# Kernel optimization log

Measured on AMD Instinct MI355X. Metric: run time of the kernel, lower is better.

## Reference

```python
import jax, jax.numpy as jnp
import numpy as np

B, S, D = 1, 2048, 1024
H, HD = 16, 64            # heads, head_dim = D // H
TEN, ED, K = 32, 128, 8   # experts, expert_dim, top_k
DS = 2048                 # shared expert dim
THETA = 10000.0
EPS = 1e-6
RSF = 2.5                 # routed_scaling_factor


def setup_inputs() -> dict:
    key = jax.random.key(0)
    ks = jax.random.split(key, 12)
    s = 0.02
    return {
        "x_input": jax.random.normal(ks[0], (B, S, D), jnp.float32),
        "indices": jax.random.randint(ks[1], (B * S, K), 0, TEN, dtype=jnp.int32),
        "values": jax.random.normal(ks[2], (B * S, K), jnp.float32),
        "w_attn": jax.random.normal(ks[3], (D, 3 * D), jnp.float32) * s,
        "w_attn_o": jax.random.normal(ks[4], (D, D), jnp.float32) * s,
        "attn_norm_w": jnp.ones((D,), jnp.float32),
        "ffn_norm_w": jnp.ones((D,), jnp.float32),
        "ffn_experts": jax.random.normal(ks[5], (3, TEN, D, ED), jnp.float32) * s,
        "keys_w": jax.random.normal(ks[6], (D, TEN), jnp.float32) * s,
        "w_up": jax.random.normal(ks[7], (D, 2 * DS), jnp.float32) * s,
        "w_down": jax.random.normal(ks[8], (DS, D), jnp.float32) * s,
    }


def rmsnorm(x, w):
    return x * jax.lax.rsqrt(jnp.mean(x * x, -1, keepdims=True) + EPS) * w


def l2norm(x):
    # F.normalize(x, dim=-1, eps=EPS)
    n = jnp.sqrt(jnp.sum(x * x, -1, keepdims=True))
    return x / jnp.maximum(n, EPS)


def rope(x):
    # x: [B, H, S, HD]
    t = jnp.arange(x.shape[2], dtype=jnp.float32)
    inv = (1.0 / THETA) ** (jnp.arange(0, HD, 2, dtype=jnp.float32) / HD)
    f = jnp.outer(t, inv)[None, None]  # [1,1,S,HD//2]
    cos, sin = jnp.cos(f), jnp.sin(f)
    x1, x2 = jnp.split(x, 2, -1)
    return jnp.concatenate([x1 * cos + x2 * sin, -x1 * sin + x2 * cos], -1)


def reference(x_input, indices, values, w_attn, w_attn_o, attn_norm_w,
              ffn_norm_w, ffn_experts, keys_w, w_up, w_down):
    # ---- attention block ----
    x = rmsnorm(x_input, attn_norm_w)
    qkv = x @ w_attn  # [B,S,3D]
    xq, xk, xv = jnp.split(qkv, 3, -1)
    to_heads = lambda t: t.reshape(B, S, H, HD).transpose(0, 2, 1, 3)  # b h s a
    xq, xk, xv = to_heads(xq), to_heads(xk), to_heads(xv)
    xq, xk = l2norm(xq), l2norm(xk)  # qk_norm
    xq, xk = rope(xq), rope(xk)
    scores = jnp.einsum('bhqd,bhkd->bhqk', xq, xk) / jnp.sqrt(jnp.float32(HD))
    causal = jnp.tril(jnp.ones((S, S), bool))
    scores = jnp.where(causal, scores, jnp.finfo(scores.dtype).min)
    probs = jax.nn.softmax(scores, -1)
    x_attn = jnp.einsum('bhqk,bhkd->bhqd', probs, xv)
    x_attn = x_attn.transpose(0, 2, 1, 3).reshape(B, S, D)
    x_attn_o = x_attn @ w_attn_o
    x_ffn_input = x_attn_o + x_input

    # ---- router ----
    x_ffn = rmsnorm(x_ffn_input, ffn_norm_w)
    xf = x_ffn.reshape(B * S, D)
    logits = xf @ keys_w  # [T, TEN]
    token_values = jnp.take_along_axis(logits, indices, -1)  # [T, K]
    gates = jax.nn.sigmoid(values + token_values) * RSF

    # ---- grouped-GEMM expert dispatch (dense equivalent: combine is linear in score) ----
    T = B * S
    w_route = jnp.zeros((T, TEN), xf.dtype).at[jnp.arange(T)[:, None], indices].add(gates)
    g = jnp.einsum('td,edh->teh', xf, ffn_experts[0])
    u = jnp.einsum('td,edh->teh', xf, ffn_experts[1])
    h = jax.nn.silu(g) * u * w_route[:, :, None]
    y = jnp.einsum('teh,edh->td', h, ffn_experts[2]).reshape(B, S, D)

    # ---- shared expert (SwiGLU FFN) ----
    x1, x2 = jnp.split(x_ffn @ w_up, 2, -1)
    y_shared = (jax.nn.silu(x1) * x2) @ w_down
    y = y + y_shared
    return y + x_ffn_input
```

## Files before the change

### kernel.cpp

```cpp
#include <hip/hip_runtime.h>
#include <math.h>

#define TOKENS 2048
#define DIM 1024
#define NHEADS 16
#define HEADDIM 64
#define NEXP 32
#define EDIM 128
#define TOPK 8
#define DSHARED 2048
#define RSF_ 2.5f
#define EPS_ 1e-6f

using bf8  = __attribute__((ext_vector_type(8))) short;
using f32x4 = __attribute__((ext_vector_type(4))) float;

__device__ __forceinline__ short f2bf(float f) {
    unsigned u = __float_as_uint(f);
    unsigned r = (u + 0x7fffu + ((u >> 16) & 1u)) >> 16;
    return (short)r;
}
__device__ __forceinline__ float bf2f(short s) {
    return __uint_as_float(((unsigned)(unsigned short)s) << 16);
}

__device__ __forceinline__ void async16(const short* g, const short* l) {
    __builtin_amdgcn_global_load_lds(
        (const __attribute__((address_space(1))) void*)(unsigned long long)g,
        (__attribute__((address_space(3))) void*)(unsigned)(unsigned long long)l,
        16, 0, 0);
}

__global__ __launch_bounds__(256) void rmsnorm_kernel(const float* __restrict__ x,
                                                      const float* __restrict__ w,
                                                      short* __restrict__ out) {
    int row = blockIdx.x;
    const float* xr = x + (long long)row * DIM;
    int t = threadIdx.x;
    float4 xv = ((const float4*)xr)[t];
    float ss = xv.x*xv.x + xv.y*xv.y + xv.z*xv.z + xv.w*xv.w;
    #pragma unroll
    for (int off = 32; off; off >>= 1) ss += __shfl_down(ss, off);
    __shared__ float warps[4];
    if ((t & 63) == 0) warps[t >> 6] = ss;
    __syncthreads();
    float tot = warps[0] + warps[1] + warps[2] + warps[3];
    float scale = rsqrtf(tot / (float)DIM + EPS_);
    float4 wv = ((const float4*)w)[t];
    short4 o;
    o.x = f2bf(xv.x * scale * wv.x);
    o.y = f2bf(xv.y * scale * wv.y);
    o.z = f2bf(xv.z * scale * wv.z);
    o.w = f2bf(xv.w * scale * wv.w);
    ((short4*)(out + (long long)row * DIM))[t] = o;
}

__global__ __launch_bounds__(256) void tconv(const float* __restrict__ in, long long sin,
                                             short* __restrict__ out, long long sout,
                                             int K, int N) {
    in  += (long long)blockIdx.z * sin;
    out += (long long)blockIdx.z * sout;
    __shared__ float t[32][33];
    int n0 = blockIdx.x * 32, k0 = blockIdx.y * 32;
    int tx = threadIdx.x & 31, ty = threadIdx.x >> 5;
    #pragma unroll
    for (int r = ty; r < 32; r += 8)
        t[r][tx] = in[(long long)(k0 + r) * N + n0 + tx];
    __syncthreads();
    #pragma unroll
    for (int r = ty; r < 32; r += 8)
        out[(long long)(n0 + r) * K + k0 + tx] = f2bf(t[tx][r]);
}

__global__ void w2conv(const float* __restrict__ in, short* __restrict__ out) {
    long long i = (long long)blockIdx.x * 256 + threadIdx.x;
    int e = (int)(i >> 17);
    int d = (int)(i >> 7) & 1023;
    int h = (int)(i & 127);
    out[(long long)d * (NEXP * EDIM) + e * EDIM + h] = f2bf(in[i]);
}

__global__ __launch_bounds__(256) void guconv(const float* __restrict__ ex,
                                              short* __restrict__ wgu) {
    int z = blockIdx.z;
    int e = z & 31, hf = z >> 5;
    const float* in = ex + (long long)hf * (NEXP * DIM * EDIM) + (long long)e * (DIM * EDIM);
    short* outp = wgu + (long long)e * (256 * 1024);
    __shared__ float t[32][33];
    int n0 = blockIdx.x * 32, k0 = blockIdx.y * 32;
    int tx = threadIdx.x & 31, ty = threadIdx.x >> 5;
    #pragma unroll
    for (int r = ty; r < 32; r += 8)
        t[r][tx] = in[(long long)(k0 + r) * EDIM + n0 + tx];
    __syncthreads();
    #pragma unroll
    for (int r = ty; r < 32; r += 8) {
        int c = n0 + r;
        int rr = ((c >> 4) << 5) + hf * 16 + (c & 15);
        outp[(long long)rr * 1024 + k0 + tx] = f2bf(t[tx][r]);
    }
}

__global__ __launch_bounds__(256) void upconv(const float* __restrict__ in,
                                              short* __restrict__ outp) {
    __shared__ float t[32][33];
    int n0 = blockIdx.x * 32, k0 = blockIdx.y * 32;
    int tx = threadIdx.x & 31, ty = threadIdx.x >> 5;
    #pragma unroll
    for (int r = ty; r < 32; r += 8)
        t[r][tx] = in[(long long)(k0 + r) * (2 * DSHARED) + n0 + tx];
    __syncthreads();
    #pragma unroll
    for (int r = ty; r < 32; r += 8) {
        int n = n0 + r;
        int hf = n >> 11, c2 = n & 2047;
        int rr = ((c2 >> 7) << 8) + (((c2 & 127) >> 4) << 5) + hf * 16 + (c2 & 15);
        outp[(long long)rr * 1024 + k0 + tx] = f2bf(t[tx][r]);
    }
}

template<int MODE>
__global__ __launch_bounds__(256) void gemm_bf16(const short* __restrict__ A, int lda, long long sA,
                                                 const short* __restrict__ Bt, int ldb, long long sBt,
                                                 void* __restrict__ Cv, int ldc, long long sC,
                                                 int M, int N, int K) {
    int koff = 0, Ksub = K;
    if (MODE >= 3) {
        Ksub = K / gridDim.z;
        koff = blockIdx.z * Ksub;
    } else {
        A  += (long long)blockIdx.z * sA;
        Bt += (long long)blockIdx.z * sBt;
    }
    float* Cf = (float*)Cv;
    short* Cs = (short*)Cv;
    Cf += (long long)blockIdx.z * sC;
    Cs += (long long)blockIdx.z * sC;
    const int m0 = blockIdx.y * 128, n0 = blockIdx.x * 128;
    __shared__ short As[128 * 64];
    __shared__ short Bs[128 * 64];
    const int tid = threadIdx.x, lane = tid & 63, w = tid >> 6;
    const int wm = (w >> 1) * 64, wn = (w & 1) * 64;
    const int drow = lane >> 3;
    const int dcol = ((lane & 7) ^ drow) * 8;
    const short* ag = A + (long long)(m0 + w * 32 + drow) * lda + koff + dcol;
    const short* bg = Bt + (long long)(n0 + w * 32 + drow) * ldb + koff + dcol;
    const short* lA = As + w * 32 * 64;
    const short* lB = Bs + w * 32 * 64;
    f32x4 acc[4][4];
    #pragma unroll
    for (int i = 0; i < 4; ++i)
        #pragma unroll
        for (int j = 0; j < 4; ++j) { f32x4 z = {0.f, 0.f, 0.f, 0.f}; acc[i][j] = z; }
    const int ra = lane & 15, quad = lane >> 4;
    const int fs0 = ((quad + 0) ^ (ra & 7)) * 8;
    const int fs1 = ((quad + 4) ^ (ra & 7)) * 8;
    for (int k0 = 0; k0 < Ksub; k0 += 64) {
        #pragma unroll
        for (int c = 0; c < 4; ++c) {
            async16(ag + (long long)(c * 8) * lda + k0, lA + c * 512);
            async16(bg + (long long)(c * 8) * ldb + k0, lB + c * 512);
        }
        __syncthreads();
        #pragma unroll
        for (int h = 0; h < 2; ++h) {
            const int fs = h ? fs1 : fs0;
            bf8 af[4], bfv[4];
            #pragma unroll
            for (int i = 0; i < 4; ++i) af[i]  = *(const bf8*)(As + (wm + i * 16 + ra) * 64 + fs);
            #pragma unroll
            for (int j = 0; j < 4; ++j) bfv[j] = *(const bf8*)(Bs + (wn + j * 16 + ra) * 64 + fs);
            #pragma unroll
            for (int i = 0; i < 4; ++i)
                #pragma unroll
                for (int j = 0; j < 4; ++j)
                    acc[i][j] = __builtin_amdgcn_mfma_f32_16x16x32_bf16(af[i], bfv[j], acc[i][j], 0, 0, 0);
        }
        __syncthreads();
    }
    const int cr = quad * 4, cc = ra;
    #pragma unroll
    for (int i = 0; i < 4; ++i) {
        #pragma unroll
        for (int r = 0; r < 4; ++r) {
            int row = m0 + wm + i * 16 + cr + r;
            long long base = (long long)row * ldc + n0 + wn + cc;
            #pragma unroll
            for (int j = 0; j < 4; ++j) {
                float v = acc[i][j][r];
                if (MODE == 2) Cs[base + j * 16] = f2bf(v);
                if (MODE == 3) Cf[base + j * 16] = v;
                if (MODE == 4) Cf[base + j * 16] = Cf[base + j * 16] + v;
            }
        }
    }
}

template<bool SCALED>
__global__ __launch_bounds__(256) void gemm_act(const short* __restrict__ A, int lda,
                                                const short* __restrict__ Bt, long long sBt,
                                                short* __restrict__ Ct, int ldct,
                                                const float* __restrict__ wr) {
    const short* Bp = Bt + (long long)blockIdx.z * sBt + (long long)blockIdx.x * (256 * 1024);
    const int cb = (blockIdx.z * gridDim.x + blockIdx.x) * 128;
    const int m0 = blockIdx.y * 64;
    __shared__ short As[2][64 * 64];
    __shared__ short Bs[2][256 * 64];
    const int tid = threadIdx.x, lane = tid & 63, w = tid >> 6;
    const int wm = (w >> 1) * 32, wn = (w & 1) * 128;
    const int drow = lane >> 3;
    const int dcol = ((lane & 7) ^ drow) * 8;
    const short* ag = A + (long long)(m0 + w * 16 + drow) * lda + dcol;
    const short* bg = Bp + (long long)(w * 64 + drow) * 1024 + dcol;
    f32x4 acc[2][8];
    #pragma unroll
    for (int i = 0; i < 2; ++i)
        #pragma unroll
        for (int j = 0; j < 8; ++j) { f32x4 z = {0.f, 0.f, 0.f, 0.f}; acc[i][j] = z; }
    const int ra = lane & 15, quad = lane >> 4;
    const int fs0 = ((quad + 0) ^ (ra & 7)) * 8;
    const int fs1 = ((quad + 4) ^ (ra & 7)) * 8;

    {
        const short* lA = As[0] + w * 16 * 64;
        const short* lB = Bs[0] + w * 64 * 64;
        async16(ag, lA);
        async16(ag + (long long)8 * lda, lA + 512);
        #pragma unroll
        for (int c = 0; c < 8; ++c)
            async16(bg + (long long)(c * 8) * 1024, lB + c * 512);
    }
    int cur = 0;
    for (int k0 = 0; k0 < 1024; k0 += 64) {
        __syncthreads();
        if (k0 + 64 < 1024) {
            const int nxt = cur ^ 1;
            const short* lA = As[nxt] + w * 16 * 64;
            const short* lB = Bs[nxt] + w * 64 * 64;
            async16(ag + k0 + 64, lA);
            async16(ag + (long long)8 * lda + k0 + 64, lA + 512);
            #pragma unroll
            for (int c = 0; c < 8; ++c)
                async16(bg + (long long)(c * 8) * 1024 + k0 + 64, lB + c * 512);
        }
        const short* cA = As[cur];
        const short* cB = Bs[cur];
        #pragma unroll
        for (int h = 0; h < 2; ++h) {
            const int fs = h ? fs1 : fs0;
            bf8 af0 = *(const bf8*)(cA + (wm + ra) * 64 + fs);
            bf8 af1 = *(const bf8*)(cA + (wm + 16 + ra) * 64 + fs);
            #pragma unroll
            for (int j = 0; j < 8; ++j) {
                bf8 bv = *(const bf8*)(cB + (wn + j * 16 + ra) * 64 + fs);
                acc[0][j] = __builtin_amdgcn_mfma_f32_16x16x32_bf16(af0, bv, acc[0][j], 0, 0, 0);
                acc[1][j] = __builtin_amdgcn_mfma_f32_16x16x32_bf16(af1, bv, acc[1][j], 0, 0, 0);
            }
        }
        cur ^= 1;
    }
    #pragma unroll
    for (int i = 0; i < 2; ++i)
        #pragma unroll
        for (int r = 0; r < 4; ++r) {
            int token = m0 + wm + i * 16 + quad * 4 + r;
            float scale = SCALED ? wr[token * NEXP + blockIdx.z] : 1.0f;
            #pragma unroll
            for (int jp = 0; jp < 4; ++jp) {
                float g = acc[i][2 * jp][r];
                float u = acc[i][2 * jp + 1][r];
                float v = g / (1.0f + __expf(-g)) * u * scale;
                Ct[(long long)token * ldct + cb + wn / 2 + jp * 16 + ra] = f2bf(v);
            }
        }
}

__global__ void combine4(const float* __restrict__ slices, const float* __restrict__ add,
                         float* __restrict__ dst) {
    long long i = (long long)blockIdx.x * 256 + threadIdx.x;
    const long long S4 = (long long)TOKENS * DIM / 4;
    float4 s = ((const float4*)add)[i];
    #pragma unroll
    for (int c = 0; c < 4; ++c) {
        float4 p = ((const float4*)slices)[c * S4 + i];
        s.x += p.x; s.y += p.y; s.z += p.z; s.w += p.w;
    }
    ((float4*)dst)[i] = s;
}

__global__ __launch_bounds__(256) void combine_rms(const float* __restrict__ slices,
                                                   const float* __restrict__ add,
                                                   const float* __restrict__ w,
                                                   float* __restrict__ xffn,
                                                   short* __restrict__ xf) {
    int row = blockIdx.x, t = threadIdx.x;
    long long i = (long long)row * 256 + t;
    const long long S4 = (long long)TOKENS * DIM / 4;
    float4 s = ((const float4*)add)[i];
    #pragma unroll
    for (int c = 0; c < 4; ++c) {
        float4 p = ((const float4*)slices)[c * S4 + i];
        s.x += p.x; s.y += p.y; s.z += p.z; s.w += p.w;
    }
    ((float4*)xffn)[i] = s;
    float ss = s.x*s.x + s.y*s.y + s.z*s.z + s.w*s.w;
    #pragma unroll
    for (int off = 32; off; off >>= 1) ss += __shfl_down(ss, off);
    __shared__ float warps[4];
    if ((t & 63) == 0) warps[t >> 6] = ss;
    __syncthreads();
    float tot = warps[0] + warps[1] + warps[2] + warps[3];
    float scale = rsqrtf(tot / (float)DIM + EPS_);
    float4 wv = ((const float4*)w)[t];
    short4 o;
    o.x = f2bf(s.x * scale * wv.x);
    o.y = f2bf(s.y * scale * wv.y);
    o.z = f2bf(s.z * scale * wv.z);
    o.w = f2bf(s.w * scale * wv.w);
    ((short4*)(xf + (long long)row * DIM))[t] = o;
}

__global__ __launch_bounds__(256) void qkv_post(const short* __restrict__ qkv,
                                                short* __restrict__ q,
                                                short* __restrict__ k) {
    int lane = threadIdx.x & 63;
    int sh = blockIdx.x * 4 + (threadIdx.x >> 6);
    int s = sh >> 4;
    int h = sh & 15;
    const short* base = qkv + (long long)s * 3 * DIM;
    float qv = bf2f(base[h * HEADDIM + lane]);
    float kv = bf2f(base[DIM + h * HEADDIM + lane]);
    float qs = qv * qv, ks = kv * kv;
    #pragma unroll
    for (int off = 32; off; off >>= 1) {
        qs += __shfl_xor(qs, off);
        ks += __shfl_xor(ks, off);
    }
    qv /= fmaxf(sqrtf(qs), EPS_);
    kv /= fmaxf(sqrtf(ks), EPS_);
    int i = lane & 31;
    float f = (float)s * powf(10000.0f, -(float)i / 32.0f);
    float c = cosf(f), sn = sinf(f);
    float qo = __shfl_xor(qv, 32);
    float ko = __shfl_xor(kv, 32);
    float sgn = (lane < 32) ? sn : -sn;
    float qr = qv * c + qo * sgn;
    float kr = kv * c + ko * sgn;
    long long o = ((long long)h * TOKENS + s) * HEADDIM + lane;
    q[o] = f2bf(qr);
    k[o] = f2bf(kr);
}

__global__ __launch_bounds__(256) void vtrans(const short* __restrict__ qkv,
                                              short* __restrict__ vt) {
    int h = blockIdx.z;
    int s0 = blockIdx.x * 32, d0 = blockIdx.y * 32;
    __shared__ short t[32][34];
    int tx = threadIdx.x & 31, ty = threadIdx.x >> 5;
    #pragma unroll
    for (int r = ty; r < 32; r += 8)
        t[r][tx] = qkv[(long long)(s0 + r) * (3 * DIM) + 2 * DIM + h * HEADDIM + d0 + tx];
    __syncthreads();
    #pragma unroll
    for (int r = ty; r < 32; r += 8)
        vt[((long long)h * HEADDIM + d0 + r) * TOKENS + s0 + tx] = t[tx][r];
}

#define PLD 68
__global__ __launch_bounds__(256) void attn_kernel(const short* __restrict__ q,
                                                   const short* __restrict__ k,
                                                   const short* __restrict__ vt,
                                                   float* __restrict__ Oacc,
                                                   float* __restrict__ lacc) {
    const int w = threadIdx.x >> 6, lane = threadIdx.x & 63;
    const int col = lane & 15, quad = lane >> 4;
    const int head = blockIdx.x / 80;
    const int t = blockIdx.x % 80;
    int qb, ch;
    if (t < 8)       { qb = t;                ch = 0; }
    else if (t < 24) { qb = 8 + (t - 8) / 2;  ch = (t - 8) % 2; }
    else if (t < 48) { qb = 16 + (t - 24) / 3; ch = (t - 24) % 3; }
    else             { qb = 24 + (t - 48) / 4; ch = (t - 48) % 4; }
    const int nch = qb / 8 + 1;
    const int ntk = qb + 1;
    const int per = (ntk + nch - 1) / nch;
    const int t0 = ch * per;
    const int t1 = (t0 + per < ntk) ? t0 + per : ntk;
    const int qbase = qb * 64 + w * 16;
    __shared__ short Ks[64 * 64];
    __shared__ short Vs[64 * 64];
    __shared__ short Ps[4 * 16 * PLD];
    short* Pw = Ps + w * 16 * PLD;
    const short* kh = k + (long long)head * TOKENS * HEADDIM;
    const short* vh = vt + (long long)head * HEADDIM * TOKENS;
    const int r8 = lane >> 3;
    const int sw = ((lane & 7) ^ r8) * 8;
    bf8 qf[2];
    #pragma unroll
    for (int ks = 0; ks < 2; ++ks)
        qf[ks] = *(const bf8*)(q + ((long long)head * TOKENS + qbase + col) * HEADDIM + ks * 32 + quad * 8);
    const int fo0 = (((0 * 4) + quad) ^ (col & 7)) * 8;
    const int fo1 = (((1 * 4) + quad) ^ (col & 7)) * 8;
    f32x4 o_[4];
    float l_[4];
    #pragma unroll
    for (int n = 0; n < 4; ++n) { f32x4 z = {0.f, 0.f, 0.f, 0.f}; o_[n] = z; }
    #pragma unroll
    for (int r = 0; r < 4; ++r) l_[r] = 0.f;
    for (int kt = t0; kt < t1; ++kt) {
        const int j0 = kt * 64;
        #pragma unroll
        for (int c = 0; c < 2; ++c) {
            int row = w * 16 + c * 8 + r8;
            async16(kh + (long long)(j0 + row) * HEADDIM + sw, Ks + (w * 16 + c * 8) * 64 + lane * 8);
            async16(vh + (long long)row * TOKENS + j0 + sw, Vs + (w * 16 + c * 8) * 64 + lane * 8);
        }
        __syncthreads();
        f32x4 sacc[4];
        #pragma unroll
        for (int n = 0; n < 4; ++n) { f32x4 z = {0.f, 0.f, 0.f, 0.f}; sacc[n] = z; }
        #pragma unroll
        for (int ks = 0; ks < 2; ++ks) {
            const int fo = ks ? fo1 : fo0;
            #pragma unroll
            for (int nt = 0; nt < 4; ++nt) {
                bf8 kf = *(const bf8*)(Ks + (nt * 16 + col) * 64 + fo);
                sacc[nt] = __builtin_amdgcn_mfma_f32_16x16x32_bf16(qf[ks], kf, sacc[nt], 0, 0, 0);
            }
        }
        const bool diag = (j0 + 64 > qbase);
        #pragma unroll
        for (int nt = 0; nt < 4; ++nt)
            #pragma unroll
            for (int r = 0; r < 4; ++r) {
                float p = __expf(sacc[nt][r] * 0.125f);
                if (diag && (j0 + nt * 16 + col > qbase + quad * 4 + r)) p = 0.f;
                l_[r] += p;
                Pw[(quad * 4 + r) * PLD + nt * 16 + col] = f2bf(p);
            }
        #pragma unroll
        for (int ks = 0; ks < 2; ++ks) {
            bf8 pf = *(const bf8*)(Pw + col * PLD + ks * 32 + quad * 8);
            const int fo = ks ? fo1 : fo0;
            #pragma unroll
            for (int nt = 0; nt < 4; ++nt) {
                bf8 vf = *(const bf8*)(Vs + (nt * 16 + col) * 64 + fo);
                o_[nt] = __builtin_amdgcn_mfma_f32_16x16x32_bf16(pf, vf, o_[nt], 0, 0, 0);
            }
        }
        __syncthreads();
    }
    float* Oc = Oacc + (long long)ch * (TOKENS * DIM);
    #pragma unroll
    for (int r = 0; r < 4; ++r) {
        int row = qbase + quad * 4 + r;
        float* op = Oc + (long long)row * DIM + head * HEADDIM;
        #pragma unroll
        for (int nt = 0; nt < 4; ++nt)
            op[nt * 16 + col] = o_[nt][r];
        float l = l_[r];
        #pragma unroll
        for (int off = 1; off < 16; off <<= 1) l += __shfl_xor(l, off);
        if (col == 0) lacc[ch * (TOKENS * NHEADS) + row * NHEADS + head] = l;
    }
}

__global__ void attn_norm(const float* __restrict__ Oacc, const float* __restrict__ lacc,
                          short* __restrict__ xo) {
    long long i = (long long)blockIdx.x * 256 + threadIdx.x;
    int row = (int)(i >> 10), col = (int)(i & 1023);
    int nch = (row >> 9) + 1;
    int head = col >> 6;
    float so = 0.f, sl = 0.f;
    for (int c = 0; c < nch; ++c) {
        so += Oacc[(long long)c * (TOKENS * DIM) + i];
        sl += lacc[c * (TOKENS * NHEADS) + row * NHEADS + head];
    }
    xo[i] = f2bf(so / sl);
}

__global__ __launch_bounds__(256) void router_kernel(const short* __restrict__ xf,
                                                     const float* __restrict__ keys_w,
                                                     const int* __restrict__ idx,
                                                     const float* __restrict__ vals,
                                                     float* __restrict__ w_route) {
    int t = blockIdx.x;
    int tid = threadIdx.x;
    int e = tid & 31, c = tid >> 5;
    const short* xr = xf + (long long)t * DIM;
    float p = 0.f;
    for (int j = 0; j < 128; ++j)
        p += bf2f(xr[c * 128 + j]) * keys_w[(c * 128 + j) * NEXP + e];
    __shared__ float part[8][32];
    part[c][e] = p;
    __syncthreads();
    if (tid < NEXP) {
        float lg = 0.f;
        #pragma unroll
        for (int cc = 0; cc < 8; ++cc) lg += part[cc][tid];
        part[0][tid] = lg;
    }
    __syncthreads();
    __shared__ float gate_s[TOPK];
    __shared__ int idx_s[TOPK];
    if (tid < TOPK) {
        int ii = idx[t * TOPK + tid];
        float g = vals[t * TOPK + tid] + part[0][ii];
        gate_s[tid] = (1.0f / (1.0f + __expf(-g))) * RSF_;
        idx_s[tid] = ii;
    }
    __syncthreads();
    if (tid < NEXP) {
        float wr = 0.f;
        #pragma unroll
        for (int kk = 0; kk < TOPK; ++kk)
            if (idx_s[kk] == tid) wr += gate_s[kk];
        w_route[(long long)t * NEXP + tid] = wr;
    }
}

extern "C" void kernel_launch(void* const* d_in, const int* in_sizes, int n_in,
                              void* d_out, int out_size, void* d_ws, size_t ws_size,
                              hipStream_t stream) {
    (void)in_sizes; (void)n_in; (void)out_size; (void)ws_size;
    const float* x_input     = (const float*)d_in[0];
    const int*   indices     = (const int*)d_in[1];
    const float* values      = (const float*)d_in[2];
    const float* w_attn      = (const float*)d_in[3];
    const float* w_attn_o    = (const float*)d_in[4];
    const float* attn_norm_w = (const float*)d_in[5];
    const float* ffn_norm_w  = (const float*)d_in[6];
    const float* ffn_experts = (const float*)d_in[7];
    const float* keys_w      = (const float*)d_in[8];
    const float* w_up        = (const float*)d_in[9];
    const float* w_down      = (const float*)d_in[10];
    float* out = (float*)d_out;
    float* ws  = (float*)d_ws;

    const long long M1 = 1024 * 1024;
    const long long SLICE = (long long)TOKENS * DIM;
    float* xffn    = ws + 0 * M1;
    short* xa_bf   = (short*)(ws + 4 * M1);
    short* xf_bf   = (short*)(ws + 4 * M1 + M1 / 2);
    short* xattn_bf= (short*)(ws + 5 * M1);
    float* w_route = ws + 5 * M1 + M1 / 2;
    float* Oacc    = ws + 6 * M1;
    float* lacc    = ws + 14 * M1;
    short* qh_bf   = (short*)(ws + 15 * M1);
    short* kh_bf   = (short*)(ws + 15 * M1 + M1 / 2);
    short* vt_bf   = (short*)(ws + 16 * M1);
    short* wattn_t = (short*)(ws + 17 * M1);
    short* wattno_t= (short*)(ws + 18 * M1 + M1 / 2);
    short* qkv_bf  = (short*)(ws + 21 * M1);
    float* oslice  = ws + 6 * M1;
    short* wgu     = (short*)(ws + 6 * M1);
    short* h_bf    = (short*)(ws + 10 * M1);
    short* w2t     = (short*)(ws + 14 * M1);
    float* yslice  = ws + 16 * M1;
    short* wupt    = (short*)(ws + 6 * M1);
    short* hs_bf   = (short*)(ws + 8 * M1);
    short* wdownt  = (short*)(ws + 10 * M1);

    tconv<<<dim3(3072 / 32, DIM / 32, 1), 256, 0, stream>>>(w_attn, 0, wattn_t, 0, DIM, 3 * DIM);
    rmsnorm_kernel<<<TOKENS, 256, 0, stream>>>(x_input, attn_norm_w, xa_bf);
    gemm_bf16<2><<<dim3(3072 / 128, TOKENS / 128, 1), 256, 0, stream>>>(
        xa_bf, DIM, 0, wattn_t, DIM, 0, qkv_bf, 3 * DIM, 0, TOKENS, 3 * DIM, DIM);
    qkv_post<<<(TOKENS * NHEADS) / 4, 256, 0, stream>>>(qkv_bf, qh_bf, kh_bf);
    vtrans<<<dim3(TOKENS / 32, HEADDIM / 32, NHEADS), 256, 0, stream>>>(qkv_bf, vt_bf);
    attn_kernel<<<NHEADS * 80, 256, 0, stream>>>(qh_bf, kh_bf, vt_bf, Oacc, lacc);
    attn_norm<<<(TOKENS * DIM) / 256, 256, 0, stream>>>(Oacc, lacc, xattn_bf);
    tconv<<<dim3(DIM / 32, DIM / 32, 1), 256, 0, stream>>>(w_attn_o, 0, wattno_t, 0, DIM, DIM);
    gemm_bf16<3><<<dim3(DIM / 128, TOKENS / 128, 4), 256, 0, stream>>>(
        xattn_bf, DIM, 0, wattno_t, DIM, 0, oslice, DIM, SLICE, TOKENS, DIM, DIM);
    combine_rms<<<TOKENS, 256, 0, stream>>>(oslice, x_input, ffn_norm_w, xffn, xf_bf);

    router_kernel<<<TOKENS, 256, 0, stream>>>(xf_bf, keys_w, indices, values, w_route);
    guconv<<<dim3(EDIM / 32, DIM / 32, 2 * NEXP), 256, 0, stream>>>(ffn_experts, wgu);
    gemm_act<true><<<dim3(1, TOKENS / 64, NEXP), 256, 0, stream>>>(
        xf_bf, DIM, wgu, 256 * 1024, h_bf, NEXP * EDIM, w_route);
    w2conv<<<(NEXP * DIM * EDIM) / 256, 256, 0, stream>>>(
        ffn_experts + 2LL * NEXP * DIM * EDIM, w2t);
    gemm_bf16<3><<<dim3(DIM / 128, TOKENS / 128, 4), 256, 0, stream>>>(
        h_bf, NEXP * EDIM, 0, w2t, NEXP * EDIM, 0, yslice, DIM, SLICE, TOKENS, DIM, NEXP * EDIM);

    upconv<<<dim3((2 * DSHARED) / 32, DIM / 32, 1), 256, 0, stream>>>(w_up, wupt);
    gemm_act<false><<<dim3((2 * DSHARED) / 256, TOKENS / 64, 1), 256, 0, stream>>>(
        xf_bf, DIM, wupt, 0, hs_bf, DSHARED, nullptr);
    tconv<<<dim3(DIM / 32, DSHARED / 32, 1), 256, 0, stream>>>(w_down, 0, wdownt, 0, DSHARED, DIM);
    gemm_bf16<4><<<dim3(DIM / 128, TOKENS / 128, 4), 256, 0, stream>>>(
        hs_bf, DSHARED, 0, wdownt, DSHARED, 0, yslice, DIM, SLICE, TOKENS, DIM, DSHARED);

    combine4<<<(TOKENS * DIM) / 1024, 256, 0, stream>>>(yslice, xffn, out);
}
```

Measured before the change: 412.5 us.

## Double-buffer LDS tiles in bf16 GEMM to overlap loads with MFMA

Shared memory tiles for A and B become two-stage ping-pong buffers. The first tile is prefetched before the loop, and each iteration issues the async load for the next K-tile right after the barrier, then computes on the current tile. This hides global-to-LDS latency behind MFMA work and removes one barrier per iteration. In exchange, LDS use per block doubles to 64KB, which can lower occupancy.

```diff
diff --git a/kernel.cpp b/kernel.cpp
--- a/kernel.cpp
+++ b/kernel.cpp
@@ -137,16 +137,14 @@
     Cf += (long long)blockIdx.z * sC;
     Cs += (long long)blockIdx.z * sC;
     const int m0 = blockIdx.y * 128, n0 = blockIdx.x * 128;
-    __shared__ short As[128 * 64];
-    __shared__ short Bs[128 * 64];
+    __shared__ short As[2][128 * 64];
+    __shared__ short Bs[2][128 * 64];
     const int tid = threadIdx.x, lane = tid & 63, w = tid >> 6;
     const int wm = (w >> 1) * 64, wn = (w & 1) * 64;
     const int drow = lane >> 3;
     const int dcol = ((lane & 7) ^ drow) * 8;
     const short* ag = A + (long long)(m0 + w * 32 + drow) * lda + koff + dcol;
     const short* bg = Bt + (long long)(n0 + w * 32 + drow) * ldb + koff + dcol;
-    const short* lA = As + w * 32 * 64;
-    const short* lB = Bs + w * 32 * 64;
     f32x4 acc[4][4];
     #pragma unroll
     for (int i = 0; i < 4; ++i)
@@ -155,28 +153,46 @@
     const int ra = lane & 15, quad = lane >> 4;
     const int fs0 = ((quad + 0) ^ (ra & 7)) * 8;
     const int fs1 = ((quad + 4) ^ (ra & 7)) * 8;
+
+    {
+        const short* lA = As[0] + w * 32 * 64;
+        const short* lB = Bs[0] + w * 32 * 64;
+        #pragma unroll
+        for (int c = 0; c < 4; ++c) {
+            async16(ag + (long long)(c * 8) * lda, lA + c * 512);
+            async16(bg + (long long)(c * 8) * ldb, lB + c * 512);
+        }
+    }
+    int cur = 0;
     for (int k0 = 0; k0 < Ksub; k0 += 64) {
-        #pragma unroll
-        for (int c = 0; c < 4; ++c) {
-            async16(ag + (long long)(c * 8) * lda + k0, lA + c * 512);
-            async16(bg + (long long)(c * 8) * ldb + k0, lB + c * 512);
-        }
         __syncthreads();
+        if (k0 + 64 < Ksub) {
+            const int nxt = cur ^ 1;
+            const short* lA = As[nxt] + w * 32 * 64;
+            const short* lB = Bs[nxt] + w * 32 * 64;
+            #pragma unroll
+            for (int c = 0; c < 4; ++c) {
+                async16(ag + (long long)(c * 8) * lda + k0 + 64, lA + c * 512);
+                async16(bg + (long long)(c * 8) * ldb + k0 + 64, lB + c * 512);
+            }
+        }
+        const short* cA = As[cur];
+        const short* cB = Bs[cur];
         #pragma unroll
         for (int h = 0; h < 2; ++h) {
             const int fs = h ? fs1 : fs0;
             bf8 af[4], bfv[4];
             #pragma unroll
-            for (int i = 0; i < 4; ++i) af[i]  = *(const bf8*)(As + (wm + i * 16 + ra) * 64 + fs);
-            #pragma unroll
-            for (int j = 0; j < 4; ++j) bfv[j] = *(const bf8*)(Bs + (wn + j * 16 + ra) * 64 + fs);
+            for (int i = 0; i < 4; ++i) af[i]  = *(const bf8*)(cA + (wm + i * 16 + ra) * 64 + fs);
+            #pragma unroll
+            for (int j = 0; j < 4; ++j) bfv[j] = *(const bf8*)(cB + (wn + j * 16 + ra) * 64 + fs);
             #pragma unroll
             for (int i = 0; i < 4; ++i)
                 #pragma unroll
                 for (int j = 0; j < 4; ++j)
                     acc[i][j] = __builtin_amdgcn_mfma_f32_16x16x32_bf16(af[i], bfv[j], acc[i][j], 0, 0, 0);
         }
-        __syncthreads();
+        cur ^= 1;
     }
     const int cr = quad * 4, cc = ra;
     #pragma unroll
```

New measurement: 395.6 us. -4.1%, faster.
